# Performance work log

Hardware: AMD Instinct MI355X
Metric: run time of the kernel (lower is better)

## Reference

```python
import jax, jax.numpy as jnp
import numpy as np

# dims: batch, seq, d_model, heads, d_ff, experts, top-k, vocab, layers
B, S, D, H, F, E, K, V, L = 2, 1024, 768, 12, 3072, 8, 2, 32000, 2
EPS = 1e-6


def setup_inputs() -> dict:
    key = jax.random.key(0)
    ks = jax.random.split(key, 12)
    n = lambda k, shape: jax.random.normal(k, shape, jnp.float32) * 0.02
    return {
        "tokens": jax.random.randint(ks[0], (B, S), 0, V),
        "emb": n(ks[1], (V, D)),            # token embedding, tied lm_head
        "pos_emb": n(ks[2], (S, D)),        # learned positions (use_rope=False)
        "wq": n(ks[3], (L, D, D)), "bq": jnp.zeros((L, D), jnp.float32),
        "wk": n(ks[4], (L, D, D)), "bk": jnp.zeros((L, D), jnp.float32),
        "wv": n(ks[5], (L, D, D)), "bv": jnp.zeros((L, D), jnp.float32),
        "wo": n(ks[6], (L, D, D)), "bo": jnp.zeros((L, D), jnp.float32),
        "ln1": jnp.ones((L, D), jnp.float32),
        "ln2": jnp.ones((L, D), jnp.float32),
        "gate_w": n(ks[7], (L, D, E)), "gate_b": jnp.zeros((L, E), jnp.float32),
        "w1": n(ks[8], (L, E, D, F)), "b1": jnp.zeros((L, E, F), jnp.float32),
        "w2": n(ks[9], (L, E, F, D)), "b2": jnp.zeros((L, E, D), jnp.float32),
        "ln_f": jnp.ones((D,), jnp.float32),
    }


def rmsnorm(x, w):
    return x * jax.lax.rsqrt(jnp.mean(x * x, axis=-1, keepdims=True) + EPS) * w


def attention(h, wq, bq, wk, bk, wv, bv, wo, bo):
    hd = D // H
    q = (h @ wq + bq).reshape(B, S, H, hd)
    k = (h @ wk + bk).reshape(B, S, H, hd)
    v = (h @ wv + bv).reshape(B, S, H, hd)
    scores = jnp.einsum('bqhd,bkhd->bhqk', q, k) / np.float32(np.sqrt(hd))
    causal = jnp.tril(jnp.ones((S, S), bool))  # mask = tril(ones(S,S))
    scores = jnp.where(causal, scores, jnp.float32(-1e9))
    probs = jax.nn.softmax(scores, axis=-1)
    out = jnp.einsum('bhqk,bkhd->bqhd', probs, v).reshape(B, S, D)
    return out @ wo + bo


def moe(h, gw, gb, w1, b1, w2, b2):
    # router: top-k over gate logits, softmax over the k selected logits
    logits = h @ gw + gb                                   # [B,S,E]
    top_vals, top_idx = jax.lax.top_k(logits, K)           # [B,S,K]
    w = jax.nn.softmax(top_vals, axis=-1)
    # combined per-expert weight = sum over capacity slots of mask*weight
    one_hot = jax.nn.one_hot(top_idx, E, dtype=h.dtype)    # [B,S,K,E]
    cw = jnp.einsum('bsk,bske->bse', w, one_hot)           # [B,S,E]
    # original computes EVERY expert's FFN on the full token batch, masks after
    h1 = jax.nn.gelu(jnp.einsum('bsd,edf->bsef', h, w1) + b1, approximate=False)
    eo = jnp.einsum('bsef,efd->bsed', h1, w2) + b2         # [B,S,E,D]
    return jnp.einsum('bsed,bse->bsd', eo, cw)


def reference(tokens, emb, pos_emb, wq, bq, wk, bk, wv, bv, wo, bo,
              ln1, ln2, gate_w, gate_b, w1, b1, w2, b2, ln_f):
    x = emb[tokens] + pos_emb[None, :S]                    # [B,S,D]
    for l in range(L):
        x = x + attention(rmsnorm(x, ln1[l]), wq[l], bq[l], wk[l], bk[l],
                          wv[l], bv[l], wo[l], bo[l])
        x = x + moe(rmsnorm(x, ln2[l]), gate_w[l], gate_b[l],
                    w1[l], b1[l], w2[l], b2[l])
    x = rmsnorm(x, ln_f)
    return x @ emb.T                                       # tied lm_head -> [B,S,V]
```

## Files before the change

### kernel.cpp

```cpp
#include <hip/hip_runtime.h>
#include <math.h>

#define TT 2048
#define BB 2
#define SS 1024
#define DD 768
#define HH 12
#define FF 3072
#define EE 8
#define VV 32000
#define NLAYER 2
#define QBLK 8

typedef __attribute__((ext_vector_type(8))) short bf16x8;
typedef __attribute__((ext_vector_type(4))) float f32x4;

#define GL16(ldst, gsrc) __builtin_amdgcn_global_load_lds( \
    (const __attribute__((address_space(1))) void*)(gsrc), \
    (__attribute__((address_space(3))) void*)(ldst), 16, 0, 0)

static __device__ __forceinline__ unsigned short f2b(float f) {
  unsigned u = __float_as_uint(f);
  unsigned r = (u + 0x7fffu + ((u >> 16) & 1u)) >> 16;
  return (unsigned short)r;
}
static __device__ __forceinline__ unsigned int pk2(float a, float b) {
  return (unsigned int)f2b(a) | ((unsigned int)f2b(b) << 16);
}

__global__ __launch_bounds__(256) void k_embed(const int* __restrict__ tok,
    const float* __restrict__ emb, const float* __restrict__ pos,
    float* __restrict__ x) {
  int t = blockIdx.x;
  int s = t & (SS - 1);
  int tk = tok[t];
  const float* er = emb + (size_t)tk * DD;
  const float* pr = pos + (size_t)s * DD;
  float* xr = x + (size_t)t * DD;
  for (int d = threadIdx.x; d < DD; d += 256)
    xr[d] = er[d] + pr[d];
}

__global__ __launch_bounds__(256) void k_rmsnorm(const float* __restrict__ x,
    const float* __restrict__ w, float* __restrict__ out,
    unsigned short* __restrict__ outb) {
  int t = blockIdx.x;
  const float* xr = x + (size_t)t * DD;
  int tid = threadIdx.x;
  float v0 = xr[tid], v1 = xr[tid + 256], v2 = xr[tid + 512];
  float ss = v0 * v0 + v1 * v1 + v2 * v2;
  for (int off = 32; off > 0; off >>= 1) ss += __shfl_down(ss, off, 64);
  __shared__ float ps[4];
  int wid = tid >> 6, lane = tid & 63;
  if (lane == 0) ps[wid] = ss;
  __syncthreads();
  float r = rsqrtf((ps[0] + ps[1] + ps[2] + ps[3]) * (1.0f / DD) + 1e-6f);
  float* orow = out + (size_t)t * DD;
  unsigned short* brow = outb + (size_t)t * DD;
  float o0 = v0 * r * w[tid], o1 = v1 * r * w[tid + 256], o2 = v2 * r * w[tid + 512];
  orow[tid] = o0; orow[tid + 256] = o1; orow[tid + 512] = o2;
  brow[tid] = f2b(o0); brow[tid + 256] = f2b(o1); brow[tid + 512] = f2b(o2);
}

__global__ __launch_bounds__(256) void k_tcvt(const float* __restrict__ src,
    unsigned short* __restrict__ dst, int R, int C, size_t srcZ, size_t dstZ) {
  src += (size_t)blockIdx.z * srcZ;
  dst += (size_t)blockIdx.z * dstZ;
  __shared__ unsigned short tile[32][40];
  int t = threadIdx.x;
  int r = t >> 3, c4 = (t & 7) * 4;
  int r0 = blockIdx.y * 32, c0 = blockIdx.x * 32;
  float4 v = *(const float4*)(src + (size_t)(r0 + r) * C + c0 + c4);
  tile[r][c4 + 0] = f2b(v.x); tile[r][c4 + 1] = f2b(v.y);
  tile[r][c4 + 2] = f2b(v.z); tile[r][c4 + 3] = f2b(v.w);
  __syncthreads();
  int cc = t >> 3, r4 = (t & 7) * 4;
  ushort4 o;
  o.x = tile[r4 + 0][cc]; o.y = tile[r4 + 1][cc];
  o.z = tile[r4 + 2][cc]; o.w = tile[r4 + 3][cc];
  *(ushort4*)(dst + (size_t)(c0 + cc) * R + r0 + r4) = o;
}

__global__ __launch_bounds__(256) void k_cvt(const float* __restrict__ src,
    unsigned short* __restrict__ dst) {
  size_t i = ((size_t)blockIdx.x * 256 + threadIdx.x) * 8;
  float4 a = *(const float4*)(src + i);
  float4 b = *(const float4*)(src + i + 4);
  ushort4 o0, o1;
  o0.x = f2b(a.x); o0.y = f2b(a.y); o0.z = f2b(a.z); o0.w = f2b(a.w);
  o1.x = f2b(b.x); o1.y = f2b(b.y); o1.z = f2b(b.z); o1.w = f2b(b.w);
  *(ushort4*)(dst + i) = o0;
  *(ushort4*)(dst + i + 4) = o1;
}

template<bool EXPERT>
__global__ __launch_bounds__(256) void k_skf32(
    const float* __restrict__ A, const float* __restrict__ W0,
    const float* __restrict__ W1, const float* __restrict__ W2,
    float* __restrict__ part, int M, int Ntot, int Nthird, int K, int KC,
    int nsplit, int prows,
    const int* __restrict__ counts, const int* __restrict__ bases) {
  int s, base = 0, cnt = M, sel = 0, n0;
  const float* W;
  if (EXPERT) {
    int z = blockIdx.z;
    s = z % nsplit;
    int e = z / nsplit;
    cnt = counts[e]; base = bases[e];
    W = W0 + (size_t)e * K * Nthird;
    n0 = blockIdx.x * 128;
  } else {
    s = blockIdx.z;
    int tpn = Nthird >> 7;
    sel = blockIdx.x / tpn;
    n0 = (blockIdx.x - sel * tpn) * 128;
    W = sel == 0 ? W0 : sel == 1 ? W1 : W2;
  }
  int m0 = blockIdx.y * 128;
  if (EXPERT && m0 >= cnt) return;
  int kbase = s * KC;

  __shared__ float As[16][132];
  __shared__ float Bs[16][132];
  int tid = threadIdx.x;
  int tx = tid & 15, ty = tid >> 4;
  int ra = tid >> 1, ka0 = (tid & 1) * 8;
  int kb = tid >> 4, nb0 = (tid & 15) * 8;
  bool arow_ok = !EXPERT || (m0 + ra < cnt);
  const float* Arow = A + (size_t)(EXPERT ? (base + m0 + (arow_ok ? ra : 0))
                                          : (m0 + ra)) * K + kbase;
  float acc[8][8] = {};

  float4 av0 = make_float4(0.f, 0.f, 0.f, 0.f), av1 = av0, bv0, bv1;
  if (arow_ok) {
    av0 = *(const float4*)(Arow + ka0);
    av1 = *(const float4*)(Arow + ka0 + 4);
  }
  {
    const float* Wrow = W + (size_t)(kbase + kb) * Nthird + n0 + nb0;
    bv0 = *(const float4*)(Wrow);
    bv1 = *(const float4*)(Wrow + 4);
  }

  for (int k0 = 0; k0 < KC; k0 += 16) {
    As[ka0 + 0][ra] = av0.x; As[ka0 + 1][ra] = av0.y;
    As[ka0 + 2][ra] = av0.z; As[ka0 + 3][ra] = av0.w;
    As[ka0 + 4][ra] = av1.x; As[ka0 + 5][ra] = av1.y;
    As[ka0 + 6][ra] = av1.z; As[ka0 + 7][ra] = av1.w;
    *(float4*)&Bs[kb][nb0] = bv0;
    *(float4*)&Bs[kb][nb0 + 4] = bv1;
    __syncthreads();
    float4 nav0 = make_float4(0.f, 0.f, 0.f, 0.f), nav1 = nav0, nbv0 = nav0, nbv1 = nav0;
    if (k0 + 16 < KC) {
      if (arow_ok) {
        nav0 = *(const float4*)(Arow + k0 + 16 + ka0);
        nav1 = *(const float4*)(Arow + k0 + 16 + ka0 + 4);
      }
      const float* Wn = W + (size_t)(kbase + k0 + 16 + kb) * Nthird + n0 + nb0;
      nbv0 = *(const float4*)(Wn);
      nbv1 = *(const float4*)(Wn + 4);
    }
#pragma unroll
    for (int kk = 0; kk < 16; kk++) {
      float4 a0 = *(const float4*)&As[kk][ty * 8];
      float4 a1 = *(const float4*)&As[kk][ty * 8 + 4];
      float4 b0 = *(const float4*)&Bs[kk][tx * 8];
      float4 b1 = *(const float4*)&Bs[kk][tx * 8 + 4];
      float a[8] = {a0.x, a0.y, a0.z, a0.w, a1.x, a1.y, a1.z, a1.w};
      float b[8] = {b0.x, b0.y, b0.z, b0.w, b1.x, b1.y, b1.z, b1.w};
#pragma unroll
      for (int i = 0; i < 8; i++) {
#pragma unroll
        for (int j = 0; j < 8; j++) acc[i][j] = fmaf(a[i], b[j], acc[i][j]);
      }
    }
    __syncthreads();
    av0 = nav0; av1 = nav1; bv0 = nbv0; bv1 = nbv1;
  }
#pragma unroll
  for (int i = 0; i < 8; i++) {
    int m = m0 + ty * 8 + i;
    if (EXPERT && m >= cnt) continue;
    size_t prow = EXPERT ? ((size_t)s * prows + base + m) : ((size_t)s * M + m);
    float* orow = part + prow * Ntot + sel * Nthird;
#pragma unroll
    for (int j = 0; j < 8; j++)
      orow[n0 + tx * 8 + j] = acc[i][j];
  }
}

__global__ __launch_bounds__(256) void k_qkvred(const float* __restrict__ part,
    const float* __restrict__ bq, const float* __restrict__ bk,
    const float* __restrict__ bv, float* __restrict__ qb,
    float* __restrict__ kb, float* __restrict__ vb) {
  int t = blockIdx.x;
  for (int c = threadIdx.x; c < 2304; c += 256) {
    float v = part[(size_t)t * 2304 + c] + part[((size_t)TT + t) * 2304 + c];
    if (c < 768)       qb[(size_t)t * DD + c] = v + bq[c];
    else if (c < 1536) kb[(size_t)t * DD + c - 768] = v + bk[c - 768];
    else               vb[(size_t)t * DD + c - 1536] = v + bv[c - 1536];
  }
}

__global__ __launch_bounds__(256) void k_ored(const float* __restrict__ part,
    const float* __restrict__ bo, float* __restrict__ x) {
  int t = blockIdx.x;
  for (int d = threadIdx.x; d < DD; d += 256) {
    float v = part[(size_t)t * DD + d]
            + part[((size_t)TT + t) * DD + d]
            + part[((size_t)2 * TT + t) * DD + d]
            + part[((size_t)3 * TT + t) * DD + d];
    x[(size_t)t * DD + d] += v + bo[d];
  }
}

__global__ __launch_bounds__(256) void k_e2red(const float* __restrict__ part,
    const int* __restrict__ rows, const int* __restrict__ tidx,
    const float* __restrict__ tw, const float* __restrict__ b2,
    float* __restrict__ x) {
  int t = blockIdx.x;
  int r0 = rows[t * 2], r1 = rows[t * 2 + 1];
  int e0 = tidx[t * 2], e1 = tidx[t * 2 + 1];
  float w0 = tw[t * 2], w1 = tw[t * 2 + 1];
  for (int d = threadIdx.x; d < DD; d += 256) {
    float v0 = part[(size_t)r0 * DD + d]
             + part[((size_t)4096 + r0) * DD + d]
             + part[((size_t)8192 + r0) * DD + d]
             + part[((size_t)12288 + r0) * DD + d] + b2[e0 * DD + d];
    float v1 = part[(size_t)r1 * DD + d]
             + part[((size_t)4096 + r1) * DD + d]
             + part[((size_t)8192 + r1) * DD + d]
             + part[((size_t)12288 + r1) * DD + d] + b2[e1 * DD + d];
    x[(size_t)t * DD + d] += w0 * v0 + w1 * v1;
  }
}

__global__ __launch_bounds__(256) void k_attn(const float* __restrict__ q,
    const float* __restrict__ k, const float* __restrict__ v, float* __restrict__ ao) {
  int b = blockIdx.z, hh = blockIdx.y, q0 = blockIdx.x * QBLK;
  __shared__ float qs[QBLK][64];
  __shared__ float sc[QBLK][SS];
  __shared__ float red[QBLK][8];
  int tid = threadIdx.x;
  const size_t hoff = (size_t)b * SS * DD + (size_t)hh * 64;
  for (int i = tid; i < QBLK * 64; i += 256) {
    int qi = i >> 6, d = i & 63;
    qs[qi][d] = q[hoff + (size_t)(q0 + qi) * DD + d];
  }
  __syncthreads();
  int kmax = q0 + QBLK;
  for (int j = tid; j < kmax; j += 256) {
    const float* kr = k + hoff + (size_t)j * DD;
    float p[QBLK];
#pragma unroll
    for (int qi = 0; qi < QBLK; qi++) p[qi] = 0.f;
#pragma unroll 4
    for (int c = 0; c < 16; c++) {
      float4 kv = *(const float4*)(kr + c * 4);
#pragma unroll
      for (int qi = 0; qi < QBLK; qi++)
        p[qi] += qs[qi][c * 4] * kv.x + qs[qi][c * 4 + 1] * kv.y +
                 qs[qi][c * 4 + 2] * kv.z + qs[qi][c * 4 + 3] * kv.w;
    }
#pragma unroll
    for (int qi = 0; qi < QBLK; qi++)
      sc[qi][j] = (j <= q0 + qi) ? p[qi] * 0.125f : -1e30f;
  }
  __syncthreads();
  int wid = tid >> 6, lane = tid & 63;
#pragma unroll
  for (int qi = 0; qi < QBLK; qi++) {
    float mx = -1e30f;
    for (int j = tid; j < kmax; j += 256) mx = fmaxf(mx, sc[qi][j]);
    for (int off = 32; off > 0; off >>= 1) mx = fmaxf(mx, __shfl_down(mx, off, 64));
    if (lane == 0) red[qi][wid] = mx;
  }
  __syncthreads();
#pragma unroll
  for (int qi = 0; qi < QBLK; qi++) {
    float mx = fmaxf(fmaxf(red[qi][0], red[qi][1]), fmaxf(red[qi][2], red[qi][3]));
    float s = 0.f;
    for (int j = tid; j < kmax; j += 256) {
      float e = __expf(sc[qi][j] - mx);
      sc[qi][j] = e;
      s += e;
    }
    for (int off = 32; off > 0; off >>= 1) s += __shfl_down(s, off, 64);
    if (lane == 0) red[qi][4 + wid] = s;
  }
  __syncthreads();
  int d = tid & 63, g = tid >> 6;
  for (int qi = g; qi < QBLK; qi += 4) {
    float inv = 1.f / (red[qi][4] + red[qi][5] + red[qi][6] + red[qi][7]);
    int jend = q0 + qi + 1;
    const float* vp = v + hoff + d;
    float a0 = 0.f, a1 = 0.f, a2 = 0.f, a3 = 0.f;
    int j = 0;
    for (; j + 4 <= jend; j += 4) {
      a0 = fmaf(sc[qi][j],     vp[(size_t)j * DD], a0);
      a1 = fmaf(sc[qi][j + 1], vp[(size_t)(j + 1) * DD], a1);
      a2 = fmaf(sc[qi][j + 2], vp[(size_t)(j + 2) * DD], a2);
      a3 = fmaf(sc[qi][j + 3], vp[(size_t)(j + 3) * DD], a3);
    }
    for (; j < jend; j++) a0 = fmaf(sc[qi][j], vp[(size_t)j * DD], a0);
    float acc = (a0 + a2) + (a1 + a3);
    ao[hoff + (size_t)(q0 + qi) * DD + d] = acc * inv;
  }
}

__global__ __launch_bounds__(256) void k_gate(const float* __restrict__ h,
    const float* __restrict__ gw, const float* __restrict__ gb,
    float* __restrict__ glog) {
  __shared__ float hr[DD];
  int t = blockIdx.x;
  for (int d = threadIdx.x; d < DD; d += 256) hr[d] = h[(size_t)t * DD + d];
  __syncthreads();
  int e = threadIdx.x >> 5, j = threadIdx.x & 31;
  float s = 0.f;
  for (int d = j; d < DD; d += 32) s += hr[d] * gw[d * EE + e];
  for (int off = 16; off > 0; off >>= 1) s += __shfl_down(s, off, 32);
  if (j == 0) glog[t * EE + e] = s + gb[e];
}

__global__ void k_zero(int* counts, int* cursor) {
  int i = threadIdx.x;
  if (i < EE) { counts[i] = 0; cursor[i] = 0; }
}

__global__ void k_router(const float* __restrict__ glog, int* __restrict__ tidx,
    float* __restrict__ tw, int* __restrict__ counts) {
  int t = blockIdx.x * 256 + threadIdx.x;
  if (t >= TT) return;
  float l[EE];
#pragma unroll
  for (int e = 0; e < EE; e++) l[e] = glog[t * EE + e];
  int i0 = 0; float v0 = l[0];
#pragma unroll
  for (int e = 1; e < EE; e++) if (l[e] > v0) { v0 = l[e]; i0 = e; }
  int i1 = -1; float v1 = -1e30f;
#pragma unroll
  for (int e = 0; e < EE; e++) if (e != i0 && l[e] > v1) { v1 = l[e]; i1 = e; }
  float e1 = __expf(v1 - v0);
  float inv = 1.f / (1.f + e1);
  tw[t * 2] = inv; tw[t * 2 + 1] = e1 * inv;
  tidx[t * 2] = i0; tidx[t * 2 + 1] = i1;
  atomicAdd(&counts[i0], 1);
  atomicAdd(&counts[i1], 1);
}

__global__ void k_scan(const int* __restrict__ counts, int* __restrict__ bases,
                       int* __restrict__ cursor) {
  int b = 0;
  for (int e = 0; e < EE; e++) { bases[e] = b; cursor[e] = b; b += counts[e]; }
}

__global__ void k_assign(const int* __restrict__ tidx, int* __restrict__ cursor,
                         int* __restrict__ rows, int* __restrict__ gtok) {
  int t = blockIdx.x * 256 + threadIdx.x;
  if (t >= TT) return;
#pragma unroll
  for (int kk = 0; kk < 2; kk++) {
    int e = tidx[t * 2 + kk];
    int r = atomicAdd(&cursor[e], 1);
    rows[t * 2 + kk] = r;
    gtok[r] = t;
  }
}

__global__ __launch_bounds__(256) void k_expert1(const float* __restrict__ h,
    const float* __restrict__ w1, const float* __restrict__ b1,
    const int* __restrict__ gtok, const int* __restrict__ counts,
    const int* __restrict__ bases, float* __restrict__ gh1) {
  int e = blockIdx.z;
  int cnt = counts[e];
  int m0 = blockIdx.y * 128;
  if (m0 >= cnt) return;
  int base = bases[e];
  int n0 = blockIdx.x * 128;
  const float* W = w1 + (size_t)e * DD * FF;
  __shared__ float As[16][132];
  __shared__ float Bs[16][132];
  int tid = threadIdx.x;
  int tx = tid & 15, ty = tid >> 4;
  int ra = tid >> 1, ka0 = (tid & 1) * 8;
  int kb = tid >> 4, nb0 = (tid & 15) * 8;
  int tok = (m0 + ra < cnt) ? gtok[base + m0 + ra] : -1;
  const float* Arow = h + (size_t)(tok < 0 ? 0 : tok) * DD;
  float acc[8][8] = {};

  float4 av0 = make_float4(0.f, 0.f, 0.f, 0.f), av1 = av0, bv0, bv1;
  if (tok >= 0) {
    av0 = *(const float4*)(Arow + ka0);
    av1 = *(const float4*)(Arow + ka0 + 4);
  }
  {
    const float* Wrow = W + (size_t)kb * FF + n0 + nb0;
    bv0 = *(const float4*)(Wrow);
    bv1 = *(const float4*)(Wrow + 4);
  }

  for (int k0 = 0; k0 < DD; k0 += 16) {
    As[ka0 + 0][ra] = av0.x; As[ka0 + 1][ra] = av0.y;
    As[ka0 + 2][ra] = av0.z; As[ka0 + 3][ra] = av0.w;
    As[ka0 + 4][ra] = av1.x; As[ka0 + 5][ra] = av1.y;
    As[ka0 + 6][ra] = av1.z; As[ka0 + 7][ra] = av1.w;
    *(float4*)&Bs[kb][nb0] = bv0;
    *(float4*)&Bs[kb][nb0 + 4] = bv1;
    __syncthreads();
    float4 nav0 = make_float4(0.f, 0.f, 0.f, 0.f), nav1 = nav0, nbv0 = nav0, nbv1 = nav0;
    if (k0 + 16 < DD) {
      if (tok >= 0) {
        nav0 = *(const float4*)(Arow + k0 + 16 + ka0);
        nav1 = *(const float4*)(Arow + k0 + 16 + ka0 + 4);
      }
      const float* Wn = W + (size_t)(k0 + 16 + kb) * FF + n0 + nb0;
      nbv0 = *(const float4*)(Wn);
      nbv1 = *(const float4*)(Wn + 4);
    }
#pragma unroll
    for (int kk = 0; kk < 16; kk++) {
      float4 a0 = *(const float4*)&As[kk][ty * 8];
      float4 a1 = *(const float4*)&As[kk][ty * 8 + 4];
      float4 b0 = *(const float4*)&Bs[kk][tx * 8];
      float4 b1 = *(const float4*)&Bs[kk][tx * 8 + 4];
      float a[8] = {a0.x, a0.y, a0.z, a0.w, a1.x, a1.y, a1.z, a1.w};
      float b[8] = {b0.x, b0.y, b0.z, b0.w, b1.x, b1.y, b1.z, b1.w};
#pragma unroll
      for (int i = 0; i < 8; i++) {
#pragma unroll
        for (int j = 0; j < 8; j++) acc[i][j] = fmaf(a[i], b[j], acc[i][j]);
      }
    }
    __syncthreads();
    av0 = nav0; av1 = nav1; bv0 = nbv0; bv1 = nbv1;
  }
#pragma unroll
  for (int i = 0; i < 8; i++) {
    int m = m0 + ty * 8 + i;
    if (m >= cnt) continue;
    float* orow = gh1 + (size_t)(base + m) * FF;
#pragma unroll
    for (int j = 0; j < 8; j++) {
      int n = n0 + tx * 8 + j;
      float vv = acc[i][j] + b1[e * FF + n];
      orow[n] = 0.5f * vv * (1.f + erff(vv * 0.70710678118654752f));
    }
  }
}

template<bool EXPERT, bool GATHER, bool BIAS, int EPI>
__global__ __launch_bounds__(256) void k_mfma2(
    const unsigned short* __restrict__ A, const unsigned short* __restrict__ Bt,
    const float* __restrict__ bias, void* __restrict__ Cv,
    int M, int N, int K,
    const int* __restrict__ gtok, const int* __restrict__ counts,
    const int* __restrict__ bases) {
  int cnt = M, base = 0;
  if (EXPERT) {
    int e = blockIdx.z;
    cnt = counts[e]; base = bases[e];
    if (BIAS) bias += (size_t)e * N;
    Bt += (size_t)e * N * K;
  }
  int m0 = blockIdx.y * 128;
  if (EXPERT && m0 >= cnt) return;
  int n0 = blockIdx.x * 128;

  __shared__ unsigned short As[128 * 32];
  __shared__ unsigned short Bs[128 * 32];

  int tid = threadIdx.x, lane = tid & 63, w = tid >> 6;
  int r0 = w * 16 + (lane >> 2);
  int r1 = 64 + r0;
  int kc = (lane & 3) * 8;

  const unsigned short *pA0, *pA1;
  if (GATHER) {
    int t0 = (m0 + r0 < cnt) ? gtok[base + m0 + r0] : 0;
    int t1 = (m0 + r1 < cnt) ? gtok[base + m0 + r1] : 0;
    pA0 = A + (size_t)t0 * K + kc;
    pA1 = A + (size_t)t1 * K + kc;
  } else if (EXPERT) {
    int q0_ = (m0 + r0 < cnt) ? base + m0 + r0 : base;
    int q1_ = (m0 + r1 < cnt) ? base + m0 + r1 : base;
    pA0 = A + (size_t)q0_ * K + kc;
    pA1 = A + (size_t)q1_ * K + kc;
  } else {
    pA0 = A + (size_t)(m0 + r0) * K + kc;
    pA1 = A + (size_t)(m0 + r1) * K + kc;
  }
  const unsigned short* pB0 = Bt + (size_t)(n0 + r0) * K + kc;
  const unsigned short* pB1 = Bt + (size_t)(n0 + r1) * K + kc;

  unsigned short* dA0 = As + w * 512;
  unsigned short* dA1 = As + 2048 + w * 512;
  unsigned short* dB0 = Bs + w * 512;
  unsigned short* dB1 = Bs + 2048 + w * 512;

  int wr = w >> 1, wc = w & 1;
  int l15 = lane & 15, lg = lane >> 4;
  const unsigned short* Ar = As + ((wr * 64 + l15) * 32 + lg * 8);
  const unsigned short* Br = Bs + ((wc * 64 + l15) * 32 + lg * 8);

  f32x4 acc[4][4];
#pragma unroll
  for (int i = 0; i < 4; i++)
#pragma unroll
    for (int j = 0; j < 4; j++) acc[i][j] = (f32x4){0.f, 0.f, 0.f, 0.f};

  for (int k0 = 0; k0 < K; k0 += 32) {
    GL16(dA0, pA0 + k0);
    GL16(dA1, pA1 + k0);
    GL16(dB0, pB0 + k0);
    GL16(dB1, pB1 + k0);
    __syncthreads();
    bf16x8 af[4], bfr[4];
#pragma unroll
    for (int f = 0; f < 4; f++) {
      af[f]  = *(const bf16x8*)(Ar + f * 512);
      bfr[f] = *(const bf16x8*)(Br + f * 512);
    }
#pragma unroll
    for (int i = 0; i < 4; i++)
#pragma unroll
      for (int j = 0; j < 4; j++)
        acc[i][j] = __builtin_amdgcn_mfma_f32_16x16x32_bf16(af[i], bfr[j], acc[i][j], 0, 0, 0);
    __syncthreads();
  }

#pragma unroll
  for (int j = 0; j < 4; j++) {
    int n = n0 + wc * 64 + j * 16 + l15;
    float bb = BIAS ? bias[n] : 0.f;
#pragma unroll
    for (int i = 0; i < 4; i++) {
      int mb = m0 + wr * 64 + i * 16 + lg * 4;
#pragma unroll
      for (int r = 0; r < 4; r++) {
        int m = mb + r;
        if (EXPERT && m >= cnt) continue;
        size_t off = (size_t)(base + m) * N + n;
        float v = acc[i][j][r] + bb;
        if (EPI == 0) {
          ((float*)Cv)[off] = v;
        } else {
          float g = 0.5f * v * (1.f + erff(v * 0.70710678118654752f));
          ((unsigned short*)Cv)[off] = f2b(g);
        }
      }
    }
  }
}

__global__ __launch_bounds__(256) void k_mfma_bf32(
    const unsigned short* __restrict__ A, const float* __restrict__ Bf,
    float* __restrict__ C, int M, int N, int K) {
  int m0 = blockIdx.y * 128;
  int n0 = blockIdx.x * 128;
  __shared__ unsigned short As[128 * 40];
  __shared__ unsigned short Bs[128 * 40];
  int tid = threadIdx.x;
  int srow = tid >> 1;
  int scol = (tid & 1) * 16;
  const unsigned short* arow = A + (size_t)(m0 + srow) * K + scol;
  const float* browf = Bf + (size_t)(n0 + srow) * K + scol;
  unsigned short* As_w = As + srow * 40 + scol;
  unsigned short* Bs_w = Bs + srow * 40 + scol;
  int lane = tid & 63, wid = tid >> 6;
  int wr = wid >> 1, wc = wid & 1;
  int l15 = lane & 15, lg = lane >> 4;
  const unsigned short* Ar = As + ((wr * 64 + l15) * 40 + lg * 8);
  const unsigned short* Br = Bs + ((wc * 64 + l15) * 40 + lg * 8);
  f32x4 acc[4][4];
#pragma unroll
  for (int i = 0; i < 4; i++)
#pragma unroll
    for (int j = 0; j < 4; j++) acc[i][j] = (f32x4){0.f, 0.f, 0.f, 0.f};
  for (int k0 = 0; k0 < K; k0 += 32) {
    uint4 av0 = *(const uint4*)(arow + k0);
    uint4 av1 = *(const uint4*)(arow + k0 + 8);
    float4 f0 = *(const float4*)(browf + k0);
    float4 f1 = *(const float4*)(browf + k0 + 4);
    float4 f2 = *(const float4*)(browf + k0 + 8);
    float4 f3 = *(const float4*)(browf + k0 + 12);
    uint4 bv0 = make_uint4(pk2(f0.x, f0.y), pk2(f0.z, f0.w), pk2(f1.x, f1.y), pk2(f1.z, f1.w));
    uint4 bv1 = make_uint4(pk2(f2.x, f2.y), pk2(f2.z, f2.w), pk2(f3.x, f3.y), pk2(f3.z, f3.w));
    *(uint4*)As_w = av0; *(uint4*)(As_w + 8) = av1;
    *(uint4*)Bs_w = bv0; *(uint4*)(Bs_w + 8) = bv1;
    __syncthreads();
    bf16x8 af[4], bfr[4];
#pragma unroll
    for (int f = 0; f < 4; f++) {
      af[f]  = *(const bf16x8*)(Ar + f * 640);
      bfr[f] = *(const bf16x8*)(Br + f * 640);
    }
#pragma unroll
    for (int i = 0; i < 4; i++)
#pragma unroll
      for (int j = 0; j < 4; j++)
        acc[i][j] = __builtin_amdgcn_mfma_f32_16x16x32_bf16(af[i], bfr[j], acc[i][j], 0, 0, 0);
    __syncthreads();
  }
#pragma unroll
  for (int j = 0; j < 4; j++) {
    int n = n0 + wc * 64 + j * 16 + l15;
#pragma unroll
    for (int i = 0; i < 4; i++) {
      int mb = m0 + wr * 64 + i * 16 + lg * 4;
#pragma unroll
      for (int r = 0; r < 4; r++)
        C[(size_t)(mb + r) * N + n] = acc[i][j][r];
    }
  }
}

__global__ __launch_bounds__(256) void k_scatter(const float* __restrict__ go,
    const int* __restrict__ rows, const float* __restrict__ tw, float* __restrict__ x) {
  int t = blockIdx.x;
  int r0 = rows[t * 2], r1 = rows[t * 2 + 1];
  float w0 = tw[t * 2], w1 = tw[t * 2 + 1];
  float* xr = x + (size_t)t * DD;
  const float* g0 = go + (size_t)r0 * DD;
  const float* g1 = go + (size_t)r1 * DD;
  for (int d = threadIdx.x; d < DD; d += 256)
    xr[d] += w0 * g0[d] + w1 * g1[d];
}

extern "C" void kernel_launch(void* const* d_in, const int* in_sizes, int n_in,
                              void* d_out, int out_size, void* d_ws, size_t ws_size,
                              hipStream_t stream) {
  (void)in_sizes; (void)n_in; (void)out_size;
  const int* tok   = (const int*)d_in[0];
  const float* emb = (const float*)d_in[1];
  const float* pos = (const float*)d_in[2];
  const float* wq  = (const float*)d_in[3];
  const float* bq  = (const float*)d_in[4];
  const float* wk  = (const float*)d_in[5];
  const float* bk  = (const float*)d_in[6];
  const float* wv  = (const float*)d_in[7];
  const float* bvv = (const float*)d_in[8];
  const float* wo  = (const float*)d_in[9];
  const float* bo  = (const float*)d_in[10];
  const float* ln1 = (const float*)d_in[11];
  const float* ln2 = (const float*)d_in[12];
  const float* gw  = (const float*)d_in[13];
  const float* gb  = (const float*)d_in[14];
  const float* w1  = (const float*)d_in[15];
  const float* b1  = (const float*)d_in[16];
  const float* w2  = (const float*)d_in[17];
  const float* b2  = (const float*)d_in[18];
  const float* lnf = (const float*)d_in[19];

  float* fp = (float*)d_out;
  float* qb   = fp; fp += (size_t)TT * DD;
  float* kb   = fp; fp += (size_t)TT * DD;
  float* vb   = fp; fp += (size_t)TT * DD;
  float* ao   = fp; fp += (size_t)TT * DD;
  float* x    = fp; fp += (size_t)TT * DD;
  float* h    = fp; fp += (size_t)TT * DD;
  float* gh1  = fp; fp += (size_t)TT * 2 * FF;
  float* go   = fp; fp += (size_t)TT * 2 * DD;
  float* glog = fp; fp += (size_t)TT * EE;
  float* tw   = fp; fp += (size_t)TT * 2;
  int* tidx   = (int*)fp; fp += TT * 2;
  int* rows   = (int*)fp; fp += TT * 2;
  int* gtok   = (int*)fp; fp += TT * 2;
  int* counts = (int*)fp; fp += 16;
  int* cursor = (int*)fp; fp += 16;
  int* bases  = (int*)fp; fp += 16;
  unsigned short* hb   = (unsigned short*)fp; fp += (size_t)TT * DD / 2;
  unsigned short* gh1b = (unsigned short*)fp; fp += (size_t)TT * 2 * FF / 2;
  unsigned short* w1t  = (unsigned short*)fp; fp += (size_t)EE * DD * FF / 2;
  unsigned short* w2t  = (unsigned short*)fp; fp += (size_t)EE * FF * DD / 2;
  float* part = fp; fp += (size_t)4 * 4096 * DD;

  unsigned short* hf = (unsigned short*)d_ws;
  unsigned short* embT = (unsigned short*)d_ws + (size_t)TT * DD;
  bool useEmbT = ws_size >= (size_t)TT * DD * 2 + (size_t)VV * DD * 2;

  k_embed<<<TT, 256, 0, stream>>>(tok, emb, pos, x);
  k_tcvt<<<dim3(96, 24, EE), 256, 0, stream>>>(w1 + (size_t)1 * EE * DD * FF, w1t,
      DD, FF, (size_t)DD * FF, (size_t)DD * FF);
  k_tcvt<<<dim3(24, 96, EE), 256, 0, stream>>>(w2 + (size_t)1 * EE * FF * DD, w2t,
      FF, DD, (size_t)FF * DD, (size_t)FF * DD);
  if (useEmbT)
    k_cvt<<<(VV * DD) / (256 * 8), 256, 0, stream>>>(emb, embT);

  for (int l = 0; l < NLAYER; l++) {
    const float* wq_l = wq + (size_t)l * DD * DD;
    const float* wk_l = wk + (size_t)l * DD * DD;
    const float* wv_l = wv + (size_t)l * DD * DD;
    const float* wo_l = wo + (size_t)l * DD * DD;

    k_rmsnorm<<<TT, 256, 0, stream>>>(x, ln1 + (size_t)l * DD, h, hb);
    k_skf32<false><<<dim3(18, 16, 2), 256, 0, stream>>>(h, wq_l, wk_l, wv_l,
        part, TT, 2304, 768, 768, 384, 2, TT, nullptr, nullptr);
    k_qkvred<<<TT, 256, 0, stream>>>(part, bq + (size_t)l * DD, bk + (size_t)l * DD,
        bvv + (size_t)l * DD, qb, kb, vb);
    k_attn<<<dim3(SS / QBLK, HH, BB), 256, 0, stream>>>(qb, kb, vb, ao);
    k_skf32<false><<<dim3(6, 16, 4), 256, 0, stream>>>(ao, wo_l, wo_l, wo_l,
        part, TT, 768, 768, 768, 192, 4, TT, nullptr, nullptr);
    k_ored<<<TT, 256, 0, stream>>>(part, bo + (size_t)l * DD, x);

    k_rmsnorm<<<TT, 256, 0, stream>>>(x, ln2 + (size_t)l * DD, h, hb);
    k_gate<<<TT, 256, 0, stream>>>(h, gw + (size_t)l * DD * EE, gb + (size_t)l * EE, glog);
    k_zero<<<1, 64, 0, stream>>>(counts, cursor);
    k_router<<<TT / 256, 256, 0, stream>>>(glog, tidx, tw, counts);
    k_scan<<<1, 1, 0, stream>>>(counts, bases, cursor);
    k_assign<<<TT / 256, 256, 0, stream>>>(tidx, cursor, rows, gtok);
    if (l < NLAYER - 1) {
      k_expert1<<<dim3(FF / 128, TT / 128, EE), 256, 0, stream>>>(
          h, w1 + (size_t)l * EE * DD * FF, b1 + (size_t)l * EE * FF,
          gtok, counts, bases, gh1);
      k_skf32<true><<<dim3(6, 16, 32), 256, 0, stream>>>(gh1,
          w2 + (size_t)l * EE * FF * DD, nullptr, nullptr,
          part, TT, 768, 768, FF, 768, 4, 4096, counts, bases);
      k_e2red<<<TT, 256, 0, stream>>>(part, rows, tidx, tw,
          b2 + (size_t)l * EE * DD, x);
    } else {
      k_mfma2<true, true, true, 2><<<dim3(FF / 128, TT / 128, EE), 256, 0, stream>>>(
          hb, w1t, b1 + (size_t)l * EE * FF, gh1b,
          TT, FF, DD, gtok, counts, bases);
      k_mfma2<true, false, true, 0><<<dim3(DD / 128, TT / 128, EE), 256, 0, stream>>>(
          gh1b, w2t, b2 + (size_t)l * EE * DD, go,
          TT, DD, FF, gtok, counts, bases);
      k_scatter<<<TT, 256, 0, stream>>>(go, rows, tw, x);
    }
  }

  k_rmsnorm<<<TT, 256, 0, stream>>>(x, lnf, h, hf);
  if (useEmbT) {
    k_mfma2<false, false, false, 0><<<dim3(VV / 128, TT / 128), 256, 0, stream>>>(
        hf, embT, nullptr, (float*)d_out,
        TT, VV, DD, nullptr, nullptr, nullptr);
  } else {
    k_mfma_bf32<<<dim3(VV / 128, TT / 128), 256, 0, stream>>>(
        hf, emb, (float*)d_out, TT, VV, DD);
  }
}
```

Baseline: 2.275 ms.

## Pair query rows in attention PV loop and stage bf16 embedding in output tail

The attention PV loop now handles two query rows per thread group in one pass, so each V load is shared by both accumulations and V memory traffic is halved. When the workspace is too small, the bf16 transposed embedding is now written into the unused tail of the output buffer (past row tile 13). The first 13 row tiles of the lm_head then run on the fast bf16 MFMA kernel, and only the last 3 row tiles use the fp32-B fallback, which overwrites that scratch region. This relies on the output tail not being read after the earlier tiles finish, and on correct launch ordering within the stream.

```diff
diff --git a/kernel.cpp b/kernel.cpp
--- a/kernel.cpp
+++ b/kernel.cpp
@@ -290,21 +290,42 @@
   }
   __syncthreads();
   int d = tid & 63, g = tid >> 6;
-  for (int qi = g; qi < QBLK; qi += 4) {
-    float inv = 1.f / (red[qi][4] + red[qi][5] + red[qi][6] + red[qi][7]);
-    int jend = q0 + qi + 1;
+  {
+    int qiA = g, qiB = g + 4;
+    float invA = 1.f / (red[qiA][4] + red[qiA][5] + red[qiA][6] + red[qiA][7]);
+    float invB = 1.f / (red[qiB][4] + red[qiB][5] + red[qiB][6] + red[qiB][7]);
+    int jendA = q0 + qiA + 1;
+    int jendB = q0 + qiB + 1;
     const float* vp = v + hoff + d;
     float a0 = 0.f, a1 = 0.f, a2 = 0.f, a3 = 0.f;
-    int j = 0;
-    for (; j + 4 <= jend; j += 4) {
-      a0 = fmaf(sc[qi][j],     vp[(size_t)j * DD], a0);
-      a1 = fmaf(sc[qi][j + 1], vp[(size_t)(j + 1) * DD], a1);
-      a2 = fmaf(sc[qi][j + 2], vp[(size_t)(j + 2) * DD], a2);
-      a3 = fmaf(sc[qi][j + 3], vp[(size_t)(j + 3) * DD], a3);
-    }
-    for (; j < jend; j++) a0 = fmaf(sc[qi][j], vp[(size_t)j * DD], a0);
-    float acc = (a0 + a2) + (a1 + a3);
-    ao[hoff + (size_t)(q0 + qi) * DD + d] = acc * inv;
+    float b0 = 0.f, b1 = 0.f, b2 = 0.f, b3 = 0.f;
+    int jA4 = jendA & ~3;
+    for (int j = 0; j < jA4; j += 4) {
+      float v0 = vp[(size_t)j * DD];
+      float v1 = vp[(size_t)(j + 1) * DD];
+      float v2 = vp[(size_t)(j + 2) * DD];
+      float v3 = vp[(size_t)(j + 3) * DD];
+      a0 = fmaf(sc[qiA][j],     v0, a0);
+      a1 = fmaf(sc[qiA][j + 1], v1, a1);
+      a2 = fmaf(sc[qiA][j + 2], v2, a2);
+      a3 = fmaf(sc[qiA][j + 3], v3, a3);
+      b0 = fmaf(sc[qiB][j],     v0, b0);
+      b1 = fmaf(sc[qiB][j + 1], v1, b1);
+      b2 = fmaf(sc[qiB][j + 2], v2, b2);
+      b3 = fmaf(sc[qiB][j + 3], v3, b3);
+    }
+    for (int t = jA4; t < jendA; t++)
+      a0 = fmaf(sc[qiA][t], vp[(size_t)t * DD], a0);
+    b0 = fmaf(sc[qiB][jA4],     vp[(size_t)jA4 * DD], b0);
+    b1 = fmaf(sc[qiB][jA4 + 1], vp[(size_t)(jA4 + 1) * DD], b1);
+    b2 = fmaf(sc[qiB][jA4 + 2], vp[(size_t)(jA4 + 2) * DD], b2);
+    b3 = fmaf(sc[qiB][jA4 + 3], vp[(size_t)(jA4 + 3) * DD], b3);
+    for (int t = jA4 + 4; t < jendB; t++)
+      b0 = fmaf(sc[qiB][t], vp[(size_t)t * DD], b0);
+    float accA = (a0 + a2) + (a1 + a3);
+    float accB = (b0 + b2) + (b1 + b3);
+    ao[hoff + (size_t)(q0 + qiA) * DD + d] = accA * invA;
+    ao[hoff + (size_t)(q0 + qiB) * DD + d] = accB * invB;
   }
 }
 
@@ -554,8 +575,8 @@
 
 __global__ __launch_bounds__(256) void k_mfma_bf32(
     const unsigned short* __restrict__ A, const float* __restrict__ Bf,
-    float* __restrict__ C, int M, int N, int K) {
-  int m0 = blockIdx.y * 128;
+    float* __restrict__ C, int M, int N, int K, int mtile0) {
+  int m0 = (blockIdx.y + mtile0) * 128;
   int n0 = blockIdx.x * 128;
   __shared__ unsigned short As[128 * 40];
   __shared__ unsigned short Bs[128 * 40];
@@ -651,7 +672,8 @@
   const float* b2  = (const float*)d_in[18];
   const float* lnf = (const float*)d_in[19];
 
-  float* fp = (float*)d_out;
+  float* ob = (float*)d_out;
+  float* fp = ob;
   float* qb   = fp; fp += (size_t)TT * DD;
   float* kb   = fp; fp += (size_t)TT * DD;
   float* vb   = fp; fp += (size_t)TT * DD;
@@ -675,16 +697,15 @@
   float* part = fp; fp += (size_t)4 * 4096 * DD;
 
   unsigned short* hf = (unsigned short*)d_ws;
-  unsigned short* embT = (unsigned short*)d_ws + (size_t)TT * DD;
-  bool useEmbT = ws_size >= (size_t)TT * DD * 2 + (size_t)VV * DD * 2;
+  bool useWs = ws_size >= (size_t)TT * DD * 2 + (size_t)VV * DD * 2;
+  unsigned short* embT = useWs ? (unsigned short*)d_ws + (size_t)TT * DD
+                               : (unsigned short*)(ob + 53248000ull);
 
   k_embed<<<TT, 256, 0, stream>>>(tok, emb, pos, x);
   k_tcvt<<<dim3(96, 24, EE), 256, 0, stream>>>(w1 + (size_t)1 * EE * DD * FF, w1t,
       DD, FF, (size_t)DD * FF, (size_t)DD * FF);
   k_tcvt<<<dim3(24, 96, EE), 256, 0, stream>>>(w2 + (size_t)1 * EE * FF * DD, w2t,
       FF, DD, (size_t)FF * DD, (size_t)FF * DD);
-  if (useEmbT)
-    k_cvt<<<(VV * DD) / (256 * 8), 256, 0, stream>>>(emb, embT);
 
   for (int l = 0; l < NLAYER; l++) {
     const float* wq_l = wq + (size_t)l * DD * DD;
@@ -728,13 +749,17 @@
     }
   }
 
+  k_cvt<<<(VV * DD) / (256 * 8), 256, 0, stream>>>(emb, embT);
   k_rmsnorm<<<TT, 256, 0, stream>>>(x, lnf, h, hf);
-  if (useEmbT) {
-    k_mfma2<false, false, false, 0><<<dim3(VV / 128, TT / 128), 256, 0, stream>>>(
+  if (useWs) {
+    k_mfma2<false, false, false, 0><<<dim3(VV / 128, 16), 256, 0, stream>>>(
         hf, embT, nullptr, (float*)d_out,
         TT, VV, DD, nullptr, nullptr, nullptr);
   } else {
-    k_mfma_bf32<<<dim3(VV / 128, TT / 128), 256, 0, stream>>>(
-        hf, emb, (float*)d_out, TT, VV, DD);
-  }
-}
+    k_mfma2<false, false, false, 0><<<dim3(VV / 128, 13), 256, 0, stream>>>(
+        hf, embT, nullptr, (float*)d_out,
+        TT, VV, DD, nullptr, nullptr, nullptr);
+    k_mfma_bf32<<<dim3(VV / 128, 3), 256, 0, stream>>>(
+        hf, emb, (float*)d_out, TT, VV, DD, 13);
+  }
+}
```

Result: faster. 2.078 ms (-8.7%).
